# Kernel tuning notes

Measured on AMD Instinct MI355X. Metric: run time of the kernel, lower is better.

The kernel has to match this reference:

```python
import jax, jax.numpy as jnp
import numpy as np
from jax import lax

N_SEEDS = 16
N_SAMPS = 32
IN_C = 3
HID = [32, 64, 64]
K = 3
H = W = 64
EPS = 1e-5


def _uniform(key, shape, bound):
    return jax.random.uniform(key, shape, jnp.float32, -bound, bound)


def setup_inputs() -> dict:
    key = jax.random.key(0)
    keys = jax.random.split(key, 32)
    inp = {"x": jax.random.normal(keys[0], (N_SEEDS, N_SAMPS, IN_C, H, W), jnp.float32)}
    c_in = IN_C
    ki = 1
    for li, c_out in enumerate(HID, start=1):
        fan_in = c_in * K * K
        # kaiming_uniform with a=sqrt(5): gain=sqrt(2/(1+5))=sqrt(1/3); bound=sqrt(3)*gain/sqrt(fan)=1/sqrt(fan)
        wb = 1.0 / np.sqrt(fan_in)
        inp[f"w{li}"] = _uniform(keys[ki], (N_SEEDS * c_out, c_in, K, K), wb); ki += 1
        inp[f"b{li}"] = _uniform(keys[ki], (N_SEEDS * c_out,), wb); ki += 1
        inp[f"g{li}"] = jnp.ones((N_SEEDS * c_out,), jnp.float32)
        inp[f"be{li}"] = jnp.zeros((N_SEEDS * c_out,), jnp.float32)
        c_in = c_out
    return inp


def _layer(h, w, b, g, be):
    # grouped conv: groups = N_SEEDS, OIHW weights, NCHW data, stride 1, pad 1
    h = lax.conv_general_dilated(
        h, w, window_strides=(1, 1), padding=((1, 1), (1, 1)),
        feature_group_count=N_SEEDS,
        dimension_numbers=("NCHW", "OIHW", "NCHW"))
    h = h + b[None, :, None, None]
    # BatchNorm2d, training mode: batch statistics over (N, H, W), biased variance
    mean = jnp.mean(h, axis=(0, 2, 3))
    var = jnp.var(h, axis=(0, 2, 3))
    h = (h - mean[None, :, None, None]) * (g / jnp.sqrt(var + EPS))[None, :, None, None] + be[None, :, None, None]
    return jax.nn.relu(h)


def reference(x, w1, b1, g1, be1, w2, b2, g2, be2, w3, b3, g3, be3):
    S, N, C, Hh, Ww = x.shape  # (n_seeds, n_samps, C, H, W)
    h = jnp.swapaxes(x, 0, 1).reshape(N, S * C, Hh, Ww)
    h = _layer(h, w1, b1, g1, be1)
    h = _layer(h, w2, b2, g2, be2)
    h = _layer(h, w3, b3, g3, be3)
    c_out = HID[-1]
    h = h.reshape(N, S, c_out, Hh, Ww)
    return jnp.swapaxes(h, 0, 1)  # (n_seeds, n_samps, C_out, H, W)
```

## Files before the change

kernel.cpp:

```cpp
#include <hip/hip_runtime.h>
#include <cstddef>
#include <cstdint>

typedef __attribute__((ext_vector_type(8))) _Float16 half8;
typedef __attribute__((ext_vector_type(4))) float f32x4;
typedef _Float16 half_t;

#define NS 16
#define NN 32

static const size_t OFF_H1P = 0;
static const size_t OFF_H2P = 138412032ull;
static const size_t OFF_ZR1 = OFF_H2P + 276824064ull;
static const size_t OFF_ZR2 = OFF_ZR1 + 67584ull;
static const size_t OFF_WT1 = OFF_ZR2 + 135168ull;
static const size_t OFF_WT2 = OFF_WT1 + 55296ull;
static const size_t OFF_WT3 = OFF_WT2 + 589824ull;
static const size_t OFF_SUMS = OFF_WT3 + 1179648ull;
static const size_t OFF_PRM = OFF_SUMS + 20480ull;
static const size_t OFF_TH  = OFF_PRM + 30720ull;

static __device__ __forceinline__ half8 sr8(half8 v, half8 t) {
    half8 r = v + t;
    half8 z = {};
#if defined(__has_builtin) && __has_builtin(__builtin_elementwise_max)
    return __builtin_elementwise_max(r, z);
#else
#pragma unroll
    for (int j = 0; j < 8; ++j) r[j] = r[j] > (_Float16)0 ? r[j] : (_Float16)0;
    return r;
#endif
}

__global__ __launch_bounds__(256) void transform1_k(
    const float* __restrict__ w1, float* __restrict__ wt1)
{
    int idx = blockIdx.x * 256 + threadIdx.x;
    if (idx >= 13824) return;
    int o = idx & 31, tap = (idx >> 5) % 9, ic = (idx / 288) % 3, s = idx / 864;
    wt1[idx] = w1[((s * 32 + o) * 3 + ic) * 9 + tap];
}

__global__ __launch_bounds__(256) void wtrans2_k(
    const float* __restrict__ w2, const float* __restrict__ a1, half_t* __restrict__ wt2)
{
    int idx = blockIdx.x * 256 + threadIdx.x;
    if (idx >= 294912) return;
    int ic = idx & 31, oc = (idx >> 5) & 63, tap = (idx >> 11) % 9, s = idx / 18432;
    wt2[idx] = (half_t)(w2[((s * 64 + oc) * 32 + ic) * 9 + tap] * a1[s * 32 + ic]);
}

__global__ __launch_bounds__(256) void wtrans3_k(
    const float* __restrict__ w3, const float* __restrict__ a2, half_t* __restrict__ wt3)
{
    int idx = blockIdx.x * 256 + threadIdx.x;
    if (idx >= 589824) return;
    int ic = idx & 63, oc = (idx >> 6) & 63, tap = (idx >> 12) % 9, s = idx / 36864;
    wt3[idx] = (half_t)(w3[((s * 64 + oc) * 64 + ic) * 9 + tap] * a2[s * 64 + ic]);
}

__global__ __launch_bounds__(256) void conv1_k(
    const float* __restrict__ x, const float* __restrict__ wt1,
    const float* __restrict__ b1, half_t* __restrict__ h1p,
    float* __restrict__ sums1)
{
    __shared__ float smem[8512];
    float* xt = smem;
    float* bounce = smem;
    float* statsl = smem + 8448;
    const int tile = blockIdx.x, s = blockIdx.y, n = blockIdx.z;
    const int tx = tile & 3, ty = tile >> 2, tid = threadIdx.x;

    for (int i = tid; i < 972; i += 256) {
        int ic = i / 324, rem = i - ic * 324;
        int py = rem / 18, px = rem - py * 18;
        int gy = ty * 16 + py - 1, gx = tx * 16 + px - 1;
        float v = 0.f;
        if ((unsigned)gy < 64u && (unsigned)gx < 64u)
            v = x[(size_t)(((s * NN + n) * 3 + ic) * 64 + gy) * 64 + gx];
        xt[i] = v;
    }
    if (tid < 64) statsl[tid] = 0.f;
    __syncthreads();

    const int px = tid & 15, py = tid >> 4;
    float acc[32];
#pragma unroll
    for (int o = 0; o < 32; ++o) acc[o] = 0.f;
#pragma unroll
    for (int ic = 0; ic < 3; ++ic)
#pragma unroll
        for (int ky = 0; ky < 3; ++ky)
#pragma unroll
            for (int kx = 0; kx < 3; ++kx) {
                float v = xt[ic * 324 + (py + ky) * 18 + px + kx];
                const float* wp = wt1 + ((s * 3 + ic) * 9 + ky * 3 + kx) * 32;
#pragma unroll
                for (int o = 0; o < 32; ++o) acc[o] = fmaf(wp[o], v, acc[o]);
            }
    const float* bp = b1 + s * 32;
#pragma unroll
    for (int o = 0; o < 32; ++o) acc[o] += bp[o];

    const int gy1 = ty * 16 + py, gxp = tx * 16 + px + 1;
    half8* dst = (half8*)(h1p + (size_t)(n * NS + s) * 135168 + (size_t)(gy1 * 66 + gxp) * 32);
#pragma unroll
    for (int k = 0; k < 4; ++k) {
        half8 v8;
#pragma unroll
        for (int j = 0; j < 8; ++j) v8[j] = (half_t)acc[k * 8 + j];
        dst[k] = v8;
    }
    __syncthreads();
#pragma unroll
    for (int o = 0; o < 32; ++o) bounce[tid * 33 + o] = acc[o];
    __syncthreads();
    {
        const int oc = tid & 31, grp = tid >> 5;
        float s1 = 0.f, s2 = 0.f;
#pragma unroll 4
        for (int j = 0; j < 32; ++j) {
            float v = bounce[(grp * 32 + j) * 33 + oc];
            s1 += v; s2 += v * v;
        }
        atomicAdd(&statsl[oc * 2], s1);
        atomicAdd(&statsl[oc * 2 + 1], s2);
    }
    __syncthreads();
    if (tid < 64)
        atomicAdd(&sums1[(s * 32 + (tid >> 1)) * 2 + (tid & 1)], statsl[tid]);
}

__global__ void bnparam_k(const float* __restrict__ sums, const float* __restrict__ g,
                          const float* __restrict__ be, float* __restrict__ a,
                          float* __restrict__ b, float* __restrict__ t,
                          half_t* __restrict__ th, int C)
{
    int ch = blockIdx.x * 256 + threadIdx.x;
    if (ch >= C) return;
    const float inv = 1.f / 131072.f;
    float mean = sums[ch * 2] * inv;
    float var = sums[ch * 2 + 1] * inv - mean * mean;
    float sc = g[ch] * rsqrtf(var + 1e-5f);
    a[ch] = sc;
    float bb = be[ch] - mean * sc;
    b[ch] = bb;
    float tt = bb / sc;
    t[ch] = tt;
    th[ch] = (half_t)tt;
}

__global__ __launch_bounds__(256) void padfill_k(
    half_t* __restrict__ img, half_t* __restrict__ zrow, const float* __restrict__ t,
    int C, int c8shift, long imgstride, int rowstride, long tot_cols, long tot)
{
    long idx = (long)blockIdx.x * 256 + threadIdx.x;
    if (idx >= tot) return;
    const int nc8m = (1 << c8shift) - 1;
    if (idx < tot_cols) {
        int c8 = (int)idx & nc8m; long r = idx >> c8shift;
        int side = (int)r & 1; r >>= 1;
        int y = (int)r & 63; r >>= 6;
        int si = (int)(r & 15); int ni = (int)(r >> 4);
        half8 q;
#pragma unroll
        for (int j = 0; j < 8; ++j) q[j] = (half_t)(-(t[si * C + c8 * 8 + j] + 1.0f));
        *(half8*)(img + (long)(ni * NS + si) * imgstride + (long)y * rowstride +
                  (side ? 65 : 0) * C + c8 * 8) = q;
    } else {
        long r2 = idx - tot_cols;
        int c8 = (int)r2 & nc8m; r2 >>= c8shift;
        int xx = (int)(r2 % 66); int si = (int)(r2 / 66);
        half8 q;
#pragma unroll
        for (int j = 0; j < 8; ++j) q[j] = (half_t)(-(t[si * C + c8 * 8 + j] + 1.0f));
        *(half8*)(zrow + ((long)(si * 66 + xx)) * C + c8 * 8) = q;
    }
}

__device__ __forceinline__ void loadB2(half8 bf[4], const half_t* wb, int tap, int l15, int g) {
#pragma unroll
    for (int nt = 0; nt < 4; ++nt)
        bf[nt] = *(const half8*)(wb + (tap * 64 + nt * 16 + l15) * 32 + g * 8);
}

__device__ __forceinline__ void comp2(f32x4 acc[4][4], const half8 bf[4], const char* smem,
                                      int tap, int wv, int l15, int g) {
    const int ky = tap / 3, kx = tap - ky * 3;
#pragma unroll
    for (int mt = 0; mt < 4; ++mt) {
        int p = (wv * 4 + mt + ky) * 18 + l15 + kx;
        half8 av = *(const half8*)(smem + p * 80 + g * 16);
#pragma unroll
        for (int nt = 0; nt < 4; ++nt)
            acc[mt][nt] = __builtin_amdgcn_mfma_f32_16x16x32_f16(av, bf[nt], acc[mt][nt], 0, 0, 0);
    }
}

__global__ __launch_bounds__(256, 3) void conv2_k(
    const half_t* __restrict__ h1p, const half_t* __restrict__ zr1,
    const half_t* __restrict__ wt2, const float* __restrict__ b2,
    const half_t* __restrict__ th1, half_t* __restrict__ h2p,
    float* __restrict__ sums2)
{
    __shared__ __align__(16) char smem[37376];
    float* statsl = (float*)(smem + 36864);
    const int tile = blockIdx.x, s = blockIdx.y, n = blockIdx.z;
    const int tx = tile & 3, ty = tile >> 2, tid = threadIdx.x;
    const int l = tid & 63, wv = tid >> 6, l15 = l & 15, g = l >> 4;
    if (tid < 128) statsl[tid] = 0.f;

    const half_t* wb = wt2 + (size_t)s * 18432;
    half8 bfa[4], bfb[4];
    loadB2(bfa, wb, 0, l15, g);

    const half_t* img = h1p + (size_t)(n * NS + s) * 135168;
    const half_t* zrow = zr1 + s * 2112;
    const int j = tid & 3;
    const half8 tshj = *(const half8*)(th1 + s * 32 + j * 8);
    for (int i = tid; i < 1296; i += 256) {
        int p = i >> 2;
        int py = p / 18, pxx = p - py * 18;
        int gy = ty * 16 + py - 1;
        const half_t* rp = ((unsigned)gy < 64u) ? (img + (size_t)gy * 2112) : zrow;
        half8 v = sr8(*(const half8*)(rp + (tx * 16 + pxx) * 32 + j * 8), tshj);
        *(half8*)(smem + p * 80 + j * 16) = v;
    }
    __syncthreads();

    f32x4 acc[4][4];
#pragma unroll
    for (int mt = 0; mt < 4; ++mt)
#pragma unroll
        for (int nt = 0; nt < 4; ++nt) acc[mt][nt] = (f32x4){0.f, 0.f, 0.f, 0.f};

#pragma unroll
    for (int tap = 0; tap < 9; ++tap) {
        if (tap & 1) {
            if (tap < 8) loadB2(bfa, wb, tap + 1, l15, g);
            comp2(acc, bfb, smem, tap, wv, l15, g);
        } else {
            if (tap < 8) loadB2(bfb, wb, tap + 1, l15, g);
            comp2(acc, bfa, smem, tap, wv, l15, g);
        }
    }

    float s1a[4], s2a[4];
#pragma unroll
    for (int nt = 0; nt < 4; ++nt) {
        float bias = b2[s * 64 + nt * 16 + l15];
        float s1 = 0.f, s2 = 0.f;
#pragma unroll
        for (int mt = 0; mt < 4; ++mt)
#pragma unroll
            for (int r = 0; r < 4; ++r) {
                float v = acc[mt][nt][r] + bias;
                acc[mt][nt][r] = v;
                s1 += v; s2 += v * v;
            }
        s1 += __shfl_xor(s1, 16); s1 += __shfl_xor(s1, 32);
        s2 += __shfl_xor(s2, 16); s2 += __shfl_xor(s2, 32);
        s1a[nt] = s1; s2a[nt] = s2;
    }
    if (l < 16) {
#pragma unroll
        for (int nt = 0; nt < 4; ++nt) {
            atomicAdd(&statsl[(nt * 16 + l15) * 2], s1a[nt]);
            atomicAdd(&statsl[(nt * 16 + l15) * 2 + 1], s2a[nt]);
        }
    }
    __syncthreads();

    half_t* obuf = (half_t*)smem;
#pragma unroll
    for (int mt = 0; mt < 4; ++mt)
#pragma unroll
        for (int nt = 0; nt < 4; ++nt)
#pragma unroll
            for (int r = 0; r < 4; ++r)
                obuf[((wv * 4 + mt) * 16 + g * 4 + r) * 72 + nt * 16 + l15] = (half_t)acc[mt][nt][r];
    __syncthreads();

    half_t* img2 = h2p + (size_t)(n * NS + s) * 270336;
    for (int i = tid; i < 2048; i += 256) {
        int p = i >> 3, cc = i & 7;
        int y = ty * 16 + (p >> 4), xp = tx * 16 + (p & 15) + 1;
        *(half8*)(img2 + (size_t)y * 4224 + xp * 64 + cc * 8) = *(const half8*)(obuf + p * 72 + cc * 8);
    }
    if (tid < 128)
        atomicAdd(&sums2[(s * 64 + (tid >> 1)) * 2 + (tid & 1)], statsl[tid]);
}

__device__ __forceinline__ void loadB3(half8 bf[2][2], const half_t* wb, int tap,
                                       int och, int l15, int g) {
#pragma unroll
    for (int nt = 0; nt < 2; ++nt) {
        const half_t* r = wb + (tap * 64 + och * 32 + nt * 16 + l15) * 64 + g * 8;
        bf[nt][0] = *(const half8*)(r);
        bf[nt][1] = *(const half8*)(r + 32);
    }
}

__device__ __forceinline__ void comp3(f32x4 acc[4][2], const half8 bf[2][2], const char* smem,
                                      int tap, int wy, int l15, int g) {
    const int ky = tap / 3, kx = tap - ky * 3;
#pragma unroll
    for (int mt = 0; mt < 4; ++mt) {
        int p = (wy + ky) * 66 + mt * 16 + l15 + kx;
        int base = p * 128, sw = (p & 7) << 4;
        half8 a0 = *(const half8*)(smem + base + ((g * 16) ^ sw));
        half8 a1 = *(const half8*)(smem + base + ((64 + g * 16) ^ sw));
#pragma unroll
        for (int nt = 0; nt < 2; ++nt) {
            acc[mt][nt] = __builtin_amdgcn_mfma_f32_16x16x32_f16(a0, bf[nt][0], acc[mt][nt], 0, 0, 0);
            acc[mt][nt] = __builtin_amdgcn_mfma_f32_16x16x32_f16(a1, bf[nt][1], acc[mt][nt], 0, 0, 0);
        }
    }
}

__global__ __launch_bounds__(512, 4) void conv3_k(
    const half_t* __restrict__ h2p, const half_t* __restrict__ zr2,
    const half_t* __restrict__ wt3, const float* __restrict__ b3,
    const half_t* __restrict__ th2, float* __restrict__ out,
    float* __restrict__ sums3)
{
    __shared__ __align__(16) char smem[51200];
    float* statsl = (float*)(smem + 50688);
    const int ty = blockIdx.x, s = blockIdx.y, n = blockIdx.z;
    const int tid = threadIdx.x;
    const int l = tid & 63, w = tid >> 6, l15 = l & 15, g = l >> 4;
    const int wy = w & 3, och = w >> 2;
    if (tid < 128) statsl[tid] = 0.f;

    const half_t* wb = wt3 + (size_t)s * 36864;
    half8 bfa[2][2], bfb[2][2];
    loadB3(bfa, wb, 0, och, l15, g);

    const half_t* img = h2p + (size_t)(n * NS + s) * 270336;
    const half_t* zrow = zr2 + s * 4224;
    const int j = tid & 7;
    const half8 tshj = *(const half8*)(th2 + s * 64 + j * 8);
    for (int i = tid; i < 3168; i += 512) {
        int p = i >> 3;
        int row = p / 66, col = p - row * 66;
        int gy = ty * 4 + row - 1;
        const half_t* rp = ((unsigned)gy < 64u) ? (img + (size_t)gy * 4224) : zrow;
        half8 v = sr8(*(const half8*)(rp + col * 64 + j * 8), tshj);
        *(half8*)(smem + p * 128 + ((j * 16) ^ ((p & 7) << 4))) = v;
    }
    __syncthreads();

    f32x4 acc[4][2];
#pragma unroll
    for (int mt = 0; mt < 4; ++mt)
#pragma unroll
        for (int nt = 0; nt < 2; ++nt) acc[mt][nt] = (f32x4){0.f, 0.f, 0.f, 0.f};

#pragma unroll
    for (int tap = 0; tap < 9; ++tap) {
        if (tap & 1) {
            if (tap < 8) loadB3(bfa, wb, tap + 1, och, l15, g);
            comp3(acc, bfb, smem, tap, wy, l15, g);
        } else {
            if (tap < 8) loadB3(bfb, wb, tap + 1, och, l15, g);
            comp3(acc, bfa, smem, tap, wy, l15, g);
        }
    }

    float s1a[2], s2a[2];
#pragma unroll
    for (int nt = 0; nt < 2; ++nt) {
        float bias = b3[s * 64 + och * 32 + nt * 16 + l15];
        float s1 = 0.f, s2 = 0.f;
#pragma unroll
        for (int mt = 0; mt < 4; ++mt)
#pragma unroll
            for (int r = 0; r < 4; ++r) {
                float v = acc[mt][nt][r] + bias;
                acc[mt][nt][r] = v;
                s1 += v; s2 += v * v;
            }
        s1 += __shfl_xor(s1, 16); s1 += __shfl_xor(s1, 32);
        s2 += __shfl_xor(s2, 16); s2 += __shfl_xor(s2, 32);
        s1a[nt] = s1; s2a[nt] = s2;
    }
    if (l < 16) {
#pragma unroll
        for (int nt = 0; nt < 2; ++nt) {
            atomicAdd(&statsl[(och * 32 + nt * 16 + l15) * 2], s1a[nt]);
            atomicAdd(&statsl[(och * 32 + nt * 16 + l15) * 2 + 1], s2a[nt]);
        }
    }

    const int gy = ty * 4 + wy;
#pragma unroll
    for (int mt = 0; mt < 4; ++mt)
#pragma unroll
        for (int nt = 0; nt < 2; ++nt) {
            int c = och * 32 + nt * 16 + l15;
            *(f32x4*)(out + ((size_t)((s * NN + n) * 64 + c) * 64 + gy) * 64 + mt * 16 + g * 4) = acc[mt][nt];
        }
    __syncthreads();
    if (tid < 128)
        atomicAdd(&sums3[(s * 64 + (tid >> 1)) * 2 + (tid & 1)], statsl[tid]);
}

__global__ __launch_bounds__(256) void final_k(float* __restrict__ out,
                                               const float* __restrict__ a3,
                                               const float* __restrict__ b3p)
{
    size_t i = ((size_t)blockIdx.x * 256 + threadIdx.x) * 4;
    int ch = (int)((i >> 12) & 63) + (int)(i >> 23) * 64;
    float sc = a3[ch], sh = b3p[ch];
    f32x4 v = *(f32x4*)(out + i);
#pragma unroll
    for (int r = 0; r < 4; ++r) v[r] = fmaxf(fmaf(sc, v[r], sh), 0.f);
    *(f32x4*)(out + i) = v;
}

extern "C" void kernel_launch(void* const* d_in, const int* in_sizes, int n_in,
                              void* d_out, int out_size, void* d_ws, size_t ws_size,
                              hipStream_t stream)
{
    const float* x   = (const float*)d_in[0];
    const float* w1  = (const float*)d_in[1];
    const float* b1  = (const float*)d_in[2];
    const float* g1  = (const float*)d_in[3];
    const float* be1 = (const float*)d_in[4];
    const float* w2  = (const float*)d_in[5];
    const float* b2  = (const float*)d_in[6];
    const float* g2  = (const float*)d_in[7];
    const float* be2 = (const float*)d_in[8];
    const float* w3  = (const float*)d_in[9];
    const float* b3  = (const float*)d_in[10];
    const float* g3  = (const float*)d_in[11];
    const float* be3 = (const float*)d_in[12];

    char* ws = (char*)d_ws;
    half_t* h1p = (half_t*)(ws + OFF_H1P);
    half_t* h2p = (half_t*)(ws + OFF_H2P);
    half_t* zr1 = (half_t*)(ws + OFF_ZR1);
    half_t* zr2 = (half_t*)(ws + OFF_ZR2);
    float*  wt1 = (float*)(ws + OFF_WT1);
    half_t* wt2 = (half_t*)(ws + OFF_WT2);
    half_t* wt3 = (half_t*)(ws + OFF_WT3);
    float*  sums = (float*)(ws + OFF_SUMS);
    float *s1v = sums, *s2v = sums + 1024, *s3v = sums + 3072;
    float*  prm = (float*)(ws + OFF_PRM);
    float *a1 = prm,        *b1p = prm + 512,  *t1 = prm + 1024;
    float *a2 = prm + 1536, *b2p = prm + 2560, *t2 = prm + 3584;
    float *a3 = prm + 4608, *b3p = prm + 5632, *t3 = prm + 6656;
    half_t* th = (half_t*)(ws + OFF_TH);
    half_t *th1 = th, *th2 = th + 512, *th3 = th + 1536;
    float* out = (float*)d_out;

    hipMemsetAsync(ws + OFF_SUMS, 0, 20480, stream);
    transform1_k<<<54, 256, 0, stream>>>(w1, wt1);
    dim3 grid(16, 16, 32);
    conv1_k<<<grid, 256, 0, stream>>>(x, wt1, b1, h1p, s1v);
    bnparam_k<<<2, 256, 0, stream>>>(s1v, g1, be1, a1, b1p, t1, th1, 512);
    padfill_k<<<1041, 256, 0, stream>>>(h1p, zr1, t1, 32, 2, 135168L, 2112, 262144L, 266368L);
    wtrans2_k<<<1152, 256, 0, stream>>>(w2, a1, wt2);
    conv2_k<<<grid, 256, 0, stream>>>(h1p, zr1, wt2, b2, th1, h2p, s2v);
    bnparam_k<<<4, 256, 0, stream>>>(s2v, g2, be2, a2, b2p, t2, th2, 1024);
    padfill_k<<<2081, 256, 0, stream>>>(h2p, zr2, t2, 64, 3, 270336L, 4224, 524288L, 532736L);
    wtrans3_k<<<2304, 256, 0, stream>>>(w3, a2, wt3);
    dim3 grid3(16, 16, 32);
    conv3_k<<<grid3, 512, 0, stream>>>(h2p, zr2, wt3, b3, th2, out, s3v);
    bnparam_k<<<4, 256, 0, stream>>>(s3v, g3, be3, a3, b3p, t3, th3, 1024);
    final_k<<<131072, 256, 0, stream>>>(out, a3, b3p);
}
```

Measured before the change: 877.0 us.

## Make conv2/conv3 blocks stream whole images through a rolling row buffer

conv2 and conv3 now launch one block per (sample, seed) image instead of many small tiles. Each block walks all 64 rows in groups of four, keeping an 8-row circular LDS buffer and prefetching the next rows into registers while the current rows compute. This removes the halo rows that were reloaded for every tile and the per-tile setup, at the cost of only 512 blocks (fewer than before) and extra barriers per row group. final_k also becomes a grid-stride loop over a smaller grid.

```diff
diff --git a/kernel.cpp b/kernel.cpp
--- a/kernel.cpp
+++ b/kernel.cpp
@@ -178,115 +178,136 @@
     }
 }
 
-__device__ __forceinline__ void loadB2(half8 bf[4], const half_t* wb, int tap, int l15, int g) {
-#pragma unroll
-    for (int nt = 0; nt < 4; ++nt)
-        bf[nt] = *(const half8*)(wb + (tap * 64 + nt * 16 + l15) * 32 + g * 8);
-}
-
-__device__ __forceinline__ void comp2(f32x4 acc[4][4], const half8 bf[4], const char* smem,
-                                      int tap, int wv, int l15, int g) {
-    const int ky = tap / 3, kx = tap - ky * 3;
+__device__ __forceinline__ void loadB2(half8 bf[2], const half_t* wb, int tap,
+                                       int och, int l15, int g) {
+#pragma unroll
+    for (int nt = 0; nt < 2; ++nt)
+        bf[nt] = *(const half8*)(wb + (tap * 64 + och * 32 + nt * 16 + l15) * 32 + g * 8);
+}
+
+__device__ __forceinline__ void comp2r(f32x4 acc[4][2], const half8 bf[2], const char* smem,
+                                       int row, int kx, int l15, int g) {
+    const char* rowp = smem + (row & 7) * 5280;
 #pragma unroll
     for (int mt = 0; mt < 4; ++mt) {
-        int p = (wv * 4 + mt + ky) * 18 + l15 + kx;
-        half8 av = *(const half8*)(smem + p * 80 + g * 16);
-#pragma unroll
-        for (int nt = 0; nt < 4; ++nt)
+        int p = mt * 16 + l15 + kx;
+        half8 av = *(const half8*)(rowp + p * 80 + g * 16);
+#pragma unroll
+        for (int nt = 0; nt < 2; ++nt)
             acc[mt][nt] = __builtin_amdgcn_mfma_f32_16x16x32_f16(av, bf[nt], acc[mt][nt], 0, 0, 0);
     }
 }
 
-__global__ __launch_bounds__(256, 3) void conv2_k(
+__global__ __launch_bounds__(512, 4) void conv2_k(
     const half_t* __restrict__ h1p, const half_t* __restrict__ zr1,
     const half_t* __restrict__ wt2, const float* __restrict__ b2,
     const half_t* __restrict__ th1, half_t* __restrict__ h2p,
     float* __restrict__ sums2)
 {
-    __shared__ __align__(16) char smem[37376];
-    float* statsl = (float*)(smem + 36864);
-    const int tile = blockIdx.x, s = blockIdx.y, n = blockIdx.z;
-    const int tx = tile & 3, ty = tile >> 2, tid = threadIdx.x;
-    const int l = tid & 63, wv = tid >> 6, l15 = l & 15, g = l >> 4;
+    __shared__ __align__(16) char smem[79616];
+    half_t* obuf = (half_t*)(smem + 42240);
+    float* statsl = (float*)(smem + 79104);
+    const int n = blockIdx.x, s = blockIdx.y;
+    const int tid = threadIdx.x;
+    const int l = tid & 63, w = tid >> 6, l15 = l & 15, g = l >> 4;
+    const int wy = w & 3, och = w >> 2;
     if (tid < 128) statsl[tid] = 0.f;
-
-    const half_t* wb = wt2 + (size_t)s * 18432;
-    half8 bfa[4], bfb[4];
-    loadB2(bfa, wb, 0, l15, g);
 
     const half_t* img = h1p + (size_t)(n * NS + s) * 135168;
     const half_t* zrow = zr1 + s * 2112;
+    const half_t* wb = wt2 + (size_t)s * 18432;
     const int j = tid & 3;
     const half8 tshj = *(const half8*)(th1 + s * 32 + j * 8);
-    for (int i = tid; i < 1296; i += 256) {
+
+    for (int i = tid; i < 1584; i += 512) {
         int p = i >> 2;
-        int py = p / 18, pxx = p - py * 18;
-        int gy = ty * 16 + py - 1;
-        const half_t* rp = ((unsigned)gy < 64u) ? (img + (size_t)gy * 2112) : zrow;
-        half8 v = sr8(*(const half8*)(rp + (tx * 16 + pxx) * 32 + j * 8), tshj);
-        *(half8*)(smem + p * 80 + j * 16) = v;
-    }
-    __syncthreads();
-
-    f32x4 acc[4][4];
-#pragma unroll
-    for (int mt = 0; mt < 4; ++mt)
-#pragma unroll
-        for (int nt = 0; nt < 4; ++nt) acc[mt][nt] = (f32x4){0.f, 0.f, 0.f, 0.f};
-
-#pragma unroll
-    for (int tap = 0; tap < 9; ++tap) {
-        if (tap & 1) {
-            if (tap < 8) loadB2(bfa, wb, tap + 1, l15, g);
-            comp2(acc, bfb, smem, tap, wv, l15, g);
-        } else {
-            if (tap < 8) loadB2(bfb, wb, tap + 1, l15, g);
-            comp2(acc, bfa, smem, tap, wv, l15, g);
+        int rr = p / 66, col = p - rr * 66;
+        int row = rr - 1;
+        const half_t* rp = (row < 0) ? zrow : (img + (size_t)row * 2112);
+        half8 v = sr8(*(const half8*)(rp + col * 32 + j * 8), tshj);
+        *(half8*)(smem + (row & 7) * 5280 + col * 80 + j * 16) = v;
+    }
+    __syncthreads();
+
+    float bias0 = b2[s * 64 + och * 32 + l15];
+    float bias1 = b2[s * 64 + och * 32 + 16 + l15];
+    float s1a0 = 0.f, s1a1 = 0.f, s2a0 = 0.f, s2a1 = 0.f;
+    half_t* img2 = h2p + (size_t)(n * NS + s) * 270336;
+
+    half8 bfa[2], bfb[2];
+#pragma unroll 1
+    for (int t = 0; t < 16; ++t) {
+        const int rowbase = 4 * t + 5;
+        half8 st0, st1, st2;
+        int sl0, sl1, sl2;
+#define PREP2(K, ST, SL) { int idx = tid + K * 512; int p = idx >> 2; int rr = p / 66; \
+        int col = p - rr * 66; int row = rowbase + rr; bool ok = (idx < 1056) && (row <= 64); \
+        const half_t* rp = (row >= 64) ? zrow : (img + (size_t)row * 2112); \
+        ST = *(const half8*)(rp + col * 32 + j * 8); \
+        SL = ok ? ((row & 7) * 5280 + col * 80 + j * 16) : -1; }
+        PREP2(0, st0, sl0)
+        PREP2(1, st1, sl1)
+        PREP2(2, st2, sl2)
+#undef PREP2
+
+        f32x4 acc[4][2];
+#pragma unroll
+        for (int mt = 0; mt < 4; ++mt)
+#pragma unroll
+            for (int nt = 0; nt < 2; ++nt) acc[mt][nt] = (f32x4){0.f, 0.f, 0.f, 0.f};
+
+        const int gy = 4 * t + wy;
+        loadB2(bfa, wb, 0, och, l15, g);
+#pragma unroll
+        for (int tap = 0; tap < 9; ++tap) {
+            int ky = tap / 3, kx = tap - ky * 3;
+            if (tap & 1) {
+                if (tap < 8) loadB2(bfa, wb, tap + 1, och, l15, g);
+                comp2r(acc, bfb, smem, gy - 1 + ky, kx, l15, g);
+            } else {
+                if (tap < 8) loadB2(bfb, wb, tap + 1, och, l15, g);
+                comp2r(acc, bfa, smem, gy - 1 + ky, kx, l15, g);
+            }
         }
-    }
-
-    float s1a[4], s2a[4];
-#pragma unroll
-    for (int nt = 0; nt < 4; ++nt) {
-        float bias = b2[s * 64 + nt * 16 + l15];
-        float s1 = 0.f, s2 = 0.f;
+
+        __syncthreads();
+        if (sl0 >= 0) *(half8*)(smem + sl0) = sr8(st0, tshj);
+        if (sl1 >= 0) *(half8*)(smem + sl1) = sr8(st1, tshj);
+        if (sl2 >= 0) *(half8*)(smem + sl2) = sr8(st2, tshj);
 #pragma unroll
         for (int mt = 0; mt < 4; ++mt)
 #pragma unroll
-            for (int r = 0; r < 4; ++r) {
-                float v = acc[mt][nt][r] + bias;
-                acc[mt][nt][r] = v;
-                s1 += v; s2 += v * v;
+            for (int nt = 0; nt < 2; ++nt) {
+                f32x4 v = acc[mt][nt];
+                float bias = nt ? bias1 : bias0;
+#pragma unroll
+                for (int r = 0; r < 4; ++r) {
+                    float vv = v[r] + bias;
+                    if (nt) { s1a1 += vv; s2a1 += vv * vv; } else { s1a0 += vv; s2a0 += vv * vv; }
+                    obuf[(wy * 64 + mt * 16 + g * 4 + r) * 72 + och * 32 + nt * 16 + l15] = (half_t)vv;
+                }
             }
-        s1 += __shfl_xor(s1, 16); s1 += __shfl_xor(s1, 32);
-        s2 += __shfl_xor(s2, 16); s2 += __shfl_xor(s2, 32);
-        s1a[nt] = s1; s2a[nt] = s2;
-    }
+        __syncthreads();
+
+        for (int i = tid; i < 2048; i += 512) {
+            int c8 = i & 7, p = i >> 3;
+            int lr = p >> 6, xx = p & 63;
+            *(half8*)(img2 + (size_t)(4 * t + lr) * 4224 + (xx + 1) * 64 + c8 * 8) =
+                *(const half8*)(obuf + p * 72 + c8 * 8);
+        }
+    }
+
+    s1a0 += __shfl_xor(s1a0, 16); s1a0 += __shfl_xor(s1a0, 32);
+    s2a0 += __shfl_xor(s2a0, 16); s2a0 += __shfl_xor(s2a0, 32);
+    s1a1 += __shfl_xor(s1a1, 16); s1a1 += __shfl_xor(s1a1, 32);
+    s2a1 += __shfl_xor(s2a1, 16); s2a1 += __shfl_xor(s2a1, 32);
     if (l < 16) {
-#pragma unroll
-        for (int nt = 0; nt < 4; ++nt) {
-            atomicAdd(&statsl[(nt * 16 + l15) * 2], s1a[nt]);
-            atomicAdd(&statsl[(nt * 16 + l15) * 2 + 1], s2a[nt]);
-        }
-    }
-    __syncthreads();
-
-    half_t* obuf = (half_t*)smem;
-#pragma unroll
-    for (int mt = 0; mt < 4; ++mt)
-#pragma unroll
-        for (int nt = 0; nt < 4; ++nt)
-#pragma unroll
-            for (int r = 0; r < 4; ++r)
-                obuf[((wv * 4 + mt) * 16 + g * 4 + r) * 72 + nt * 16 + l15] = (half_t)acc[mt][nt][r];
-    __syncthreads();
-
-    half_t* img2 = h2p + (size_t)(n * NS + s) * 270336;
-    for (int i = tid; i < 2048; i += 256) {
-        int p = i >> 3, cc = i & 7;
-        int y = ty * 16 + (p >> 4), xp = tx * 16 + (p & 15) + 1;
-        *(half8*)(img2 + (size_t)y * 4224 + xp * 64 + cc * 8) = *(const half8*)(obuf + p * 72 + cc * 8);
-    }
+        atomicAdd(&statsl[(och * 32 + l15) * 2], s1a0);
+        atomicAdd(&statsl[(och * 32 + l15) * 2 + 1], s2a0);
+        atomicAdd(&statsl[(och * 32 + 16 + l15) * 2], s1a1);
+        atomicAdd(&statsl[(och * 32 + 16 + l15) * 2 + 1], s2a1);
+    }
+    __syncthreads();
     if (tid < 128)
         atomicAdd(&sums2[(s * 64 + (tid >> 1)) * 2 + (tid & 1)], statsl[tid]);
 }
@@ -301,15 +322,15 @@
     }
 }
 
-__device__ __forceinline__ void comp3(f32x4 acc[4][2], const half8 bf[2][2], const char* smem,
-                                      int tap, int wy, int l15, int g) {
-    const int ky = tap / 3, kx = tap - ky * 3;
+__device__ __forceinline__ void comp3r(f32x4 acc[4][2], const half8 bf[2][2], const char* smem,
+                                       int row, int kx, int l15, int g) {
+    const char* rowp = smem + (row & 7) * 8448;
 #pragma unroll
     for (int mt = 0; mt < 4; ++mt) {
-        int p = (wy + ky) * 66 + mt * 16 + l15 + kx;
+        int p = mt * 16 + l15 + kx;
         int base = p * 128, sw = (p & 7) << 4;
-        half8 a0 = *(const half8*)(smem + base + ((g * 16) ^ sw));
-        half8 a1 = *(const half8*)(smem + base + ((64 + g * 16) ^ sw));
+        half8 a0 = *(const half8*)(rowp + base + ((g * 16) ^ sw));
+        half8 a1 = *(const half8*)(rowp + base + ((64 + g * 16) ^ sw));
 #pragma unroll
         for (int nt = 0; nt < 2; ++nt) {
             acc[mt][nt] = __builtin_amdgcn_mfma_f32_16x16x32_f16(a0, bf[nt][0], acc[mt][nt], 0, 0, 0);
@@ -324,82 +345,109 @@
     const half_t* __restrict__ th2, float* __restrict__ out,
     float* __restrict__ sums3)
 {
-    __shared__ __align__(16) char smem[51200];
-    float* statsl = (float*)(smem + 50688);
-    const int ty = blockIdx.x, s = blockIdx.y, n = blockIdx.z;
+    __shared__ __align__(16) char smem[68096];
+    float* statsl = (float*)(smem + 67584);
+    const int n = blockIdx.x, s = blockIdx.y;
     const int tid = threadIdx.x;
     const int l = tid & 63, w = tid >> 6, l15 = l & 15, g = l >> 4;
     const int wy = w & 3, och = w >> 2;
     if (tid < 128) statsl[tid] = 0.f;
 
-    const half_t* wb = wt3 + (size_t)s * 36864;
-    half8 bfa[2][2], bfb[2][2];
-    loadB3(bfa, wb, 0, och, l15, g);
-
     const half_t* img = h2p + (size_t)(n * NS + s) * 270336;
     const half_t* zrow = zr2 + s * 4224;
+    const half_t* wb = wt3 + (size_t)s * 36864;
     const int j = tid & 7;
     const half8 tshj = *(const half8*)(th2 + s * 64 + j * 8);
+
     for (int i = tid; i < 3168; i += 512) {
         int p = i >> 3;
-        int row = p / 66, col = p - row * 66;
-        int gy = ty * 4 + row - 1;
-        const half_t* rp = ((unsigned)gy < 64u) ? (img + (size_t)gy * 4224) : zrow;
+        int rr = p / 66, col = p - rr * 66;
+        int row = rr - 1;
+        const half_t* rp = (row < 0) ? zrow : (img + (size_t)row * 4224);
         half8 v = sr8(*(const half8*)(rp + col * 64 + j * 8), tshj);
-        *(half8*)(smem + p * 128 + ((j * 16) ^ ((p & 7) << 4))) = v;
-    }
-    __syncthreads();
-
-    f32x4 acc[4][2];
-#pragma unroll
-    for (int mt = 0; mt < 4; ++mt)
-#pragma unroll
-        for (int nt = 0; nt < 2; ++nt) acc[mt][nt] = (f32x4){0.f, 0.f, 0.f, 0.f};
-
-#pragma unroll
-    for (int tap = 0; tap < 9; ++tap) {
-        if (tap & 1) {
-            if (tap < 8) loadB3(bfa, wb, tap + 1, och, l15, g);
-            comp3(acc, bfb, smem, tap, wy, l15, g);
-        } else {
-            if (tap < 8) loadB3(bfb, wb, tap + 1, och, l15, g);
-            comp3(acc, bfa, smem, tap, wy, l15, g);
+        *(half8*)(smem + (row & 7) * 8448 + col * 128 + ((j * 16) ^ ((col & 7) << 4))) = v;
+    }
+    __syncthreads();
+
+    float bias0 = b3[s * 64 + och * 32 + l15];
+    float bias1 = b3[s * 64 + och * 32 + 16 + l15];
+    float s1a0 = 0.f, s1a1 = 0.f, s2a0 = 0.f, s2a1 = 0.f;
+    const size_t obase = (size_t)((s * NN + n) * 64) * 4096;
+
+    half8 bfa[2][2], bfb[2][2];
+#pragma unroll 1
+    for (int t = 0; t < 16; ++t) {
+        const int rowbase = 4 * t + 5;
+        half8 st0, st1, st2, st3, st4;
+        int sl0, sl1, sl2, sl3, sl4;
+#define PREP3(K, ST, SL) { int idx = tid + K * 512; int p = idx >> 3; int rr = p / 66; \
+        int col = p - rr * 66; int row = rowbase + rr; bool ok = (idx < 2112) && (row <= 64); \
+        const half_t* rp = (row >= 64) ? zrow : (img + (size_t)row * 4224); \
+        ST = *(const half8*)(rp + col * 64 + j * 8); \
+        SL = ok ? ((row & 7) * 8448 + col * 128 + ((j * 16) ^ ((col & 7) << 4))) : -1; }
+        PREP3(0, st0, sl0)
+        PREP3(1, st1, sl1)
+        PREP3(2, st2, sl2)
+        PREP3(3, st3, sl3)
+        PREP3(4, st4, sl4)
+#undef PREP3
+
+        f32x4 acc[4][2];
+#pragma unroll
+        for (int mt = 0; mt < 4; ++mt)
+#pragma unroll
+            for (int nt = 0; nt < 2; ++nt) acc[mt][nt] = (f32x4){0.f, 0.f, 0.f, 0.f};
+
+        const int gy = 4 * t + wy;
+        loadB3(bfa, wb, 0, och, l15, g);
+#pragma unroll
+        for (int tap = 0; tap < 9; ++tap) {
+            int ky = tap / 3, kx = tap - ky * 3;
+            if (tap & 1) {
+                if (tap < 8) loadB3(bfa, wb, tap + 1, och, l15, g);
+                comp3r(acc, bfb, smem, gy - 1 + ky, kx, l15, g);
+            } else {
+                if (tap < 8) loadB3(bfb, wb, tap + 1, och, l15, g);
+                comp3r(acc, bfa, smem, gy - 1 + ky, kx, l15, g);
+            }
         }
-    }
-
-    float s1a[2], s2a[2];
-#pragma unroll
-    for (int nt = 0; nt < 2; ++nt) {
-        float bias = b3[s * 64 + och * 32 + nt * 16 + l15];
-        float s1 = 0.f, s2 = 0.f;
-#pragma unroll
-        for (int mt = 0; mt < 4; ++mt)
-#pragma unroll
-            for (int r = 0; r < 4; ++r) {
-                float v = acc[mt][nt][r] + bias;
-                acc[mt][nt][r] = v;
-                s1 += v; s2 += v * v;
-            }
-        s1 += __shfl_xor(s1, 16); s1 += __shfl_xor(s1, 32);
-        s2 += __shfl_xor(s2, 16); s2 += __shfl_xor(s2, 32);
-        s1a[nt] = s1; s2a[nt] = s2;
-    }
-    if (l < 16) {
-#pragma unroll
-        for (int nt = 0; nt < 2; ++nt) {
-            atomicAdd(&statsl[(och * 32 + nt * 16 + l15) * 2], s1a[nt]);
-            atomicAdd(&statsl[(och * 32 + nt * 16 + l15) * 2 + 1], s2a[nt]);
-        }
-    }
-
-    const int gy = ty * 4 + wy;
-#pragma unroll
-    for (int mt = 0; mt < 4; ++mt)
+
 #pragma unroll
         for (int nt = 0; nt < 2; ++nt) {
             int c = och * 32 + nt * 16 + l15;
-            *(f32x4*)(out + ((size_t)((s * NN + n) * 64 + c) * 64 + gy) * 64 + mt * 16 + g * 4) = acc[mt][nt];
+            float bias = nt ? bias1 : bias0;
+#pragma unroll
+            for (int mt = 0; mt < 4; ++mt) {
+                f32x4 v = acc[mt][nt];
+#pragma unroll
+                for (int r = 0; r < 4; ++r) {
+                    float vv = v[r] + bias;
+                    v[r] = vv;
+                    if (nt) { s1a1 += vv; s2a1 += vv * vv; } else { s1a0 += vv; s2a0 += vv * vv; }
+                }
+                *(f32x4*)(out + obase + (size_t)c * 4096 + gy * 64 + mt * 16 + g * 4) = v;
+            }
         }
+
+        __syncthreads();
+        if (sl0 >= 0) *(half8*)(smem + sl0) = sr8(st0, tshj);
+        if (sl1 >= 0) *(half8*)(smem + sl1) = sr8(st1, tshj);
+        if (sl2 >= 0) *(half8*)(smem + sl2) = sr8(st2, tshj);
+        if (sl3 >= 0) *(half8*)(smem + sl3) = sr8(st3, tshj);
+        if (sl4 >= 0) *(half8*)(smem + sl4) = sr8(st4, tshj);
+        __syncthreads();
+    }
+
+    s1a0 += __shfl_xor(s1a0, 16); s1a0 += __shfl_xor(s1a0, 32);
+    s2a0 += __shfl_xor(s2a0, 16); s2a0 += __shfl_xor(s2a0, 32);
+    s1a1 += __shfl_xor(s1a1, 16); s1a1 += __shfl_xor(s1a1, 32);
+    s2a1 += __shfl_xor(s2a1, 16); s2a1 += __shfl_xor(s2a1, 32);
+    if (l < 16) {
+        atomicAdd(&statsl[(och * 32 + l15) * 2], s1a0);
+        atomicAdd(&statsl[(och * 32 + l15) * 2 + 1], s2a0);
+        atomicAdd(&statsl[(och * 32 + 16 + l15) * 2], s1a1);
+        atomicAdd(&statsl[(och * 32 + 16 + l15) * 2 + 1], s2a1);
+    }
     __syncthreads();
     if (tid < 128)
         atomicAdd(&sums3[(s * 64 + (tid >> 1)) * 2 + (tid & 1)], statsl[tid]);
@@ -409,13 +457,16 @@
                                                const float* __restrict__ a3,
                                                const float* __restrict__ b3p)
 {
-    size_t i = ((size_t)blockIdx.x * 256 + threadIdx.x) * 4;
-    int ch = (int)((i >> 12) & 63) + (int)(i >> 23) * 64;
-    float sc = a3[ch], sh = b3p[ch];
-    f32x4 v = *(f32x4*)(out + i);
-#pragma unroll
-    for (int r = 0; r < 4; ++r) v[r] = fmaxf(fmaf(sc, v[r], sh), 0.f);
-    *(f32x4*)(out + i) = v;
+    const size_t stride = (size_t)gridDim.x * 256;
+    for (size_t i = (size_t)blockIdx.x * 256 + threadIdx.x; i < 33554432ull; i += stride) {
+        size_t e = i * 4;
+        int ch = (int)((e >> 12) & 63) + (int)(e >> 23) * 64;
+        float sc = a3[ch], sh = b3p[ch];
+        f32x4 v = *(f32x4*)(out + e);
+#pragma unroll
+        for (int r = 0; r < 4; ++r) v[r] = fmaxf(fmaf(sc, v[r], sh), 0.f);
+        *(f32x4*)(out + e) = v;
+    }
 }
 
 extern "C" void kernel_launch(void* const* d_in, const int* in_sizes, int n_in,
@@ -456,17 +507,17 @@
 
     hipMemsetAsync(ws + OFF_SUMS, 0, 20480, stream);
     transform1_k<<<54, 256, 0, stream>>>(w1, wt1);
-    dim3 grid(16, 16, 32);
-    conv1_k<<<grid, 256, 0, stream>>>(x, wt1, b1, h1p, s1v);
+    dim3 grid1(16, 16, 32);
+    conv1_k<<<grid1, 256, 0, stream>>>(x, wt1, b1, h1p, s1v);
     bnparam_k<<<2, 256, 0, stream>>>(s1v, g1, be1, a1, b1p, t1, th1, 512);
     padfill_k<<<1041, 256, 0, stream>>>(h1p, zr1, t1, 32, 2, 135168L, 2112, 262144L, 266368L);
     wtrans2_k<<<1152, 256, 0, stream>>>(w2, a1, wt2);
-    conv2_k<<<grid, 256, 0, stream>>>(h1p, zr1, wt2, b2, th1, h2p, s2v);
+    dim3 gridr(32, 16);
+    conv2_k<<<gridr, 512, 0, stream>>>(h1p, zr1, wt2, b2, th1, h2p, s2v);
     bnparam_k<<<4, 256, 0, stream>>>(s2v, g2, be2, a2, b2p, t2, th2, 1024);
     padfill_k<<<2081, 256, 0, stream>>>(h2p, zr2, t2, 64, 3, 270336L, 4224, 524288L, 532736L);
     wtrans3_k<<<2304, 256, 0, stream>>>(w3, a2, wt3);
-    dim3 grid3(16, 16, 32);
-    conv3_k<<<grid3, 512, 0, stream>>>(h2p, zr2, wt3, b3, th2, out, s3v);
+    conv3_k<<<gridr, 512, 0, stream>>>(h2p, zr2, wt3, b3, th2, out, s3v);
     bnparam_k<<<4, 256, 0, stream>>>(s3v, g3, be3, a3, b3p, t3, th3, 1024);
-    final_k<<<131072, 256, 0, stream>>>(out, a3, b3p);
-}
+    final_k<<<4096, 256, 0, stream>>>(out, a3, b3p);
+}
```

Measured after the change: 1.298 ms. 48.0% more time.

## Split layer-3 input channels into two halves to shrink LDS and overlap staging

Applied to the files above, without the earlier changes.

Intermediate h2 is stored as two 32-channel planes instead of one interleaved 64-channel image, with matching changes to the conv2 store and a new padfill3 kernel. conv3 now stages one 32-channel half in LDS at a time, loading the second half into registers while the first half's MFMAs run. This cuts LDS from about 51 KB to 32 KB and raises the launch-bounds occupancy hint from 4 to 6. Bias and statistics are now fused into the output store, and final_k becomes a grid-stride loop with fewer blocks. The costs are extra barriers, more register pressure from the prefetched halves, and dropping the XOR swizzle in favour of an 80-byte padded stride.

```diff
diff --git a/kernel.cpp b/kernel.cpp
--- a/kernel.cpp
+++ b/kernel.cpp
@@ -119,8 +119,8 @@
         const int oc = tid & 31, grp = tid >> 5;
         float s1 = 0.f, s2 = 0.f;
 #pragma unroll 4
-        for (int j = 0; j < 32; ++j) {
-            float v = bounce[(grp * 32 + j) * 33 + oc];
+        for (int jj = 0; jj < 32; ++jj) {
+            float v = bounce[(grp * 32 + jj) * 33 + oc];
             s1 += v; s2 += v * v;
         }
         atomicAdd(&statsl[oc * 2], s1);
@@ -178,6 +178,34 @@
     }
 }
 
+__global__ __launch_bounds__(256) void padfill3_k(
+    half_t* __restrict__ h2p, half_t* __restrict__ zr2, const float* __restrict__ t)
+{
+    int idx = blockIdx.x * 256 + threadIdx.x;
+    if (idx >= 532736) return;
+    if (idx < 524288) {
+        int c8 = idx & 3; int r = idx >> 2;
+        int side = r & 1; r >>= 1;
+        int y = r & 63; r >>= 6;
+        int kc = r & 1; r >>= 1;
+        int si = r & 15; int ni = r >> 4;
+        half8 q;
+#pragma unroll
+        for (int j = 0; j < 8; ++j) q[j] = (half_t)(-(t[si * 64 + kc * 32 + c8 * 8 + j] + 1.0f));
+        *(half8*)(h2p + (size_t)(ni * NS + si) * 270336 + kc * 135168 +
+                  (size_t)y * 2112 + (side ? 65 : 0) * 32 + c8 * 8) = q;
+    } else {
+        int r2 = idx - 524288;
+        int c8 = r2 & 3; r2 >>= 2;
+        int xx = r2 % 66; r2 /= 66;
+        int kc = r2 & 1; int si = r2 >> 1;
+        half8 q;
+#pragma unroll
+        for (int j = 0; j < 8; ++j) q[j] = (half_t)(-(t[si * 64 + kc * 32 + c8 * 8 + j] + 1.0f));
+        *(half8*)(zr2 + si * 4224 + kc * 2112 + xx * 32 + c8 * 8) = q;
+    }
+}
+
 __device__ __forceinline__ void loadB2(half8 bf[4], const half_t* wb, int tap, int l15, int g) {
 #pragma unroll
     for (int nt = 0; nt < 4; ++nt)
@@ -283,72 +311,61 @@
 
     half_t* img2 = h2p + (size_t)(n * NS + s) * 270336;
     for (int i = tid; i < 2048; i += 256) {
-        int p = i >> 3, cc = i & 7;
+        int c8 = i & 3, p = (i >> 2) & 255, kc = i >> 10;
         int y = ty * 16 + (p >> 4), xp = tx * 16 + (p & 15) + 1;
-        *(half8*)(img2 + (size_t)y * 4224 + xp * 64 + cc * 8) = *(const half8*)(obuf + p * 72 + cc * 8);
+        *(half8*)(img2 + kc * 135168 + (size_t)y * 2112 + xp * 32 + c8 * 8) =
+            *(const half8*)(obuf + p * 72 + kc * 32 + c8 * 8);
     }
     if (tid < 128)
         atomicAdd(&sums2[(s * 64 + (tid >> 1)) * 2 + (tid & 1)], statsl[tid]);
 }
 
-__device__ __forceinline__ void loadB3(half8 bf[2][2], const half_t* wb, int tap,
-                                       int och, int l15, int g) {
-#pragma unroll
-    for (int nt = 0; nt < 2; ++nt) {
-        const half_t* r = wb + (tap * 64 + och * 32 + nt * 16 + l15) * 64 + g * 8;
-        bf[nt][0] = *(const half8*)(r);
-        bf[nt][1] = *(const half8*)(r + 32);
-    }
-}
-
-__device__ __forceinline__ void comp3(f32x4 acc[4][2], const half8 bf[2][2], const char* smem,
-                                      int tap, int wy, int l15, int g) {
-    const int ky = tap / 3, kx = tap - ky * 3;
-#pragma unroll
-    for (int mt = 0; mt < 4; ++mt) {
-        int p = (wy + ky) * 66 + mt * 16 + l15 + kx;
-        int base = p * 128, sw = (p & 7) << 4;
-        half8 a0 = *(const half8*)(smem + base + ((g * 16) ^ sw));
-        half8 a1 = *(const half8*)(smem + base + ((64 + g * 16) ^ sw));
-#pragma unroll
-        for (int nt = 0; nt < 2; ++nt) {
-            acc[mt][nt] = __builtin_amdgcn_mfma_f32_16x16x32_f16(a0, bf[nt][0], acc[mt][nt], 0, 0, 0);
-            acc[mt][nt] = __builtin_amdgcn_mfma_f32_16x16x32_f16(a1, bf[nt][1], acc[mt][nt], 0, 0, 0);
-        }
-    }
-}
-
-__global__ __launch_bounds__(512, 4) void conv3_k(
+__global__ __launch_bounds__(512, 6) void conv3_k(
     const half_t* __restrict__ h2p, const half_t* __restrict__ zr2,
     const half_t* __restrict__ wt3, const float* __restrict__ b3,
     const half_t* __restrict__ th2, float* __restrict__ out,
     float* __restrict__ sums3)
 {
-    __shared__ __align__(16) char smem[51200];
-    float* statsl = (float*)(smem + 50688);
+    __shared__ __align__(16) char smem[32192];
+    float* statsl = (float*)(smem + 31680);
     const int ty = blockIdx.x, s = blockIdx.y, n = blockIdx.z;
     const int tid = threadIdx.x;
     const int l = tid & 63, w = tid >> 6, l15 = l & 15, g = l >> 4;
     const int wy = w & 3, och = w >> 2;
+    const int ty4 = ty * 4;
     if (tid < 128) statsl[tid] = 0.f;
 
+    const half_t* img0 = h2p + (size_t)(n * NS + s) * 270336;
+    const half_t* img1 = img0 + 135168;
+    const half_t* zr0 = zr2 + s * 4224;
+    const half_t* zr1p = zr0 + 2112;
     const half_t* wb = wt3 + (size_t)s * 36864;
-    half8 bfa[2][2], bfb[2][2];
-    loadB3(bfa, wb, 0, och, l15, g);
-
-    const half_t* img = h2p + (size_t)(n * NS + s) * 270336;
-    const half_t* zrow = zr2 + s * 4224;
-    const int j = tid & 7;
-    const half8 tshj = *(const half8*)(th2 + s * 64 + j * 8);
-    for (int i = tid; i < 3168; i += 512) {
-        int p = i >> 3;
-        int row = p / 66, col = p - row * 66;
-        int gy = ty * 4 + row - 1;
-        const half_t* rp = ((unsigned)gy < 64u) ? (img + (size_t)gy * 4224) : zrow;
-        half8 v = sr8(*(const half8*)(rp + col * 64 + j * 8), tshj);
-        *(half8*)(smem + p * 128 + ((j * 16) ^ ((p & 7) << 4))) = v;
-    }
-    __syncthreads();
+    const int j = tid & 3;
+    const half8 tsh0 = *(const half8*)(th2 + s * 64 + j * 8);
+    const half8 tsh1 = *(const half8*)(th2 + s * 64 + 32 + j * 8);
+
+    half8 sa0, sa1, sa2, sa3; int aa0, aa1, aa2, aa3;
+#define PREP(K, ST, SL, IMG, ZR) { int idx = tid + K * 512; int p = idx >> 2; int rr = p / 66; \
+    int col = p - rr * 66; int row = ty4 - 1 + rr; bool okk = idx < 1584; \
+    const half_t* rp = ((unsigned)row < 64u) ? ((IMG) + (size_t)row * 2112) : (ZR); \
+    ST = *(const half8*)(rp + col * 32 + j * 8); \
+    SL = okk ? (rr * 5280 + col * 80 + j * 16) : -1; }
+    PREP(0, sa0, aa0, img0, zr0)
+    PREP(1, sa1, aa1, img0, zr0)
+    PREP(2, sa2, aa2, img0, zr0)
+    PREP(3, sa3, aa3, img0, zr0)
+    if (aa0 >= 0) *(half8*)(smem + aa0) = sr8(sa0, tsh0);
+    if (aa1 >= 0) *(half8*)(smem + aa1) = sr8(sa1, tsh0);
+    if (aa2 >= 0) *(half8*)(smem + aa2) = sr8(sa2, tsh0);
+    if (aa3 >= 0) *(half8*)(smem + aa3) = sr8(sa3, tsh0);
+    __syncthreads();
+
+    half8 sb0, sb1, sb2, sb3; int ab0, ab1, ab2, ab3;
+    PREP(0, sb0, ab0, img1, zr1p)
+    PREP(1, sb1, ab1, img1, zr1p)
+    PREP(2, sb2, ab2, img1, zr1p)
+    PREP(3, sb3, ab3, img1, zr1p)
+#undef PREP
 
     f32x4 acc[4][2];
 #pragma unroll
@@ -356,50 +373,93 @@
 #pragma unroll
         for (int nt = 0; nt < 2; ++nt) acc[mt][nt] = (f32x4){0.f, 0.f, 0.f, 0.f};
 
-#pragma unroll
-    for (int tap = 0; tap < 9; ++tap) {
-        if (tap & 1) {
-            if (tap < 8) loadB3(bfa, wb, tap + 1, och, l15, g);
-            comp3(acc, bfb, smem, tap, wy, l15, g);
-        } else {
-            if (tap < 8) loadB3(bfb, wb, tap + 1, och, l15, g);
-            comp3(acc, bfa, smem, tap, wy, l15, g);
-        }
-    }
-
-    float s1a[2], s2a[2];
-#pragma unroll
-    for (int nt = 0; nt < 2; ++nt) {
-        float bias = b3[s * 64 + och * 32 + nt * 16 + l15];
-        float s1 = 0.f, s2 = 0.f;
-#pragma unroll
-        for (int mt = 0; mt < 4; ++mt)
-#pragma unroll
-            for (int r = 0; r < 4; ++r) {
-                float v = acc[mt][nt][r] + bias;
-                acc[mt][nt][r] = v;
-                s1 += v; s2 += v * v;
-            }
-        s1 += __shfl_xor(s1, 16); s1 += __shfl_xor(s1, 32);
-        s2 += __shfl_xor(s2, 16); s2 += __shfl_xor(s2, 32);
-        s1a[nt] = s1; s2a[nt] = s2;
-    }
-    if (l < 16) {
-#pragma unroll
-        for (int nt = 0; nt < 2; ++nt) {
-            atomicAdd(&statsl[(och * 32 + nt * 16 + l15) * 2], s1a[nt]);
-            atomicAdd(&statsl[(och * 32 + nt * 16 + l15) * 2 + 1], s2a[nt]);
-        }
-    }
-
-    const int gy = ty * 4 + wy;
+    half8 bqa[2], bqb[2];
+#define LWA(TAP, KC) { \
+    bqa[0] = *(const half8*)(wb + ((TAP) * 64 + och * 32 + l15) * 64 + (KC) * 32 + g * 8); \
+    bqa[1] = *(const half8*)(wb + ((TAP) * 64 + och * 32 + 16 + l15) * 64 + (KC) * 32 + g * 8); }
+#define LWB(TAP, KC) { \
+    bqb[0] = *(const half8*)(wb + ((TAP) * 64 + och * 32 + l15) * 64 + (KC) * 32 + g * 8); \
+    bqb[1] = *(const half8*)(wb + ((TAP) * 64 + och * 32 + 16 + l15) * 64 + (KC) * 32 + g * 8); }
+#define CSA(KY, KX) { const char* rp_ = smem + (wy + (KY)) * 5280; \
+    _Pragma("unroll") \
+    for (int mt = 0; mt < 4; ++mt) { \
+        int px = mt * 16 + l15 + (KX); \
+        half8 a_ = *(const half8*)(rp_ + px * 80 + g * 16); \
+        acc[mt][0] = __builtin_amdgcn_mfma_f32_16x16x32_f16(a_, bqa[0], acc[mt][0], 0, 0, 0); \
+        acc[mt][1] = __builtin_amdgcn_mfma_f32_16x16x32_f16(a_, bqa[1], acc[mt][1], 0, 0, 0); \
+    } }
+#define CSB(KY, KX) { const char* rp_ = smem + (wy + (KY)) * 5280; \
+    _Pragma("unroll") \
+    for (int mt = 0; mt < 4; ++mt) { \
+        int px = mt * 16 + l15 + (KX); \
+        half8 a_ = *(const half8*)(rp_ + px * 80 + g * 16); \
+        acc[mt][0] = __builtin_amdgcn_mfma_f32_16x16x32_f16(a_, bqb[0], acc[mt][0], 0, 0, 0); \
+        acc[mt][1] = __builtin_amdgcn_mfma_f32_16x16x32_f16(a_, bqb[1], acc[mt][1], 0, 0, 0); \
+    } }
+
+    LWA(0, 0)
+    LWB(1, 0)  CSA(0, 0)
+    LWA(2, 0)  CSB(0, 1)
+    LWB(3, 0)  CSA(0, 2)
+    LWA(4, 0)  CSB(1, 0)
+    LWB(5, 0)  CSA(1, 1)
+    LWA(6, 0)  CSB(1, 2)
+    LWB(7, 0)  CSA(2, 0)
+    LWA(8, 0)  CSB(2, 1)
+    LWB(0, 1)  CSA(2, 2)
+    __syncthreads();
+
+    if (ab0 >= 0) *(half8*)(smem + ab0) = sr8(sb0, tsh1);
+    if (ab1 >= 0) *(half8*)(smem + ab1) = sr8(sb1, tsh1);
+    if (ab2 >= 0) *(half8*)(smem + ab2) = sr8(sb2, tsh1);
+    if (ab3 >= 0) *(half8*)(smem + ab3) = sr8(sb3, tsh1);
+    __syncthreads();
+
+    LWA(1, 1)  CSB(0, 0)
+    LWB(2, 1)  CSA(0, 1)
+    LWA(3, 1)  CSB(0, 2)
+    LWB(4, 1)  CSA(1, 0)
+    LWA(5, 1)  CSB(1, 1)
+    LWB(6, 1)  CSA(1, 2)
+    LWA(7, 1)  CSB(2, 0)
+    LWB(8, 1)  CSA(2, 1)
+               CSB(2, 2)
+#undef CSA
+#undef CSB
+#undef LWA
+#undef LWB
+
+    float bias0 = b3[s * 64 + och * 32 + l15];
+    float bias1 = b3[s * 64 + och * 32 + 16 + l15];
+    float s10 = 0.f, s20 = 0.f, s11 = 0.f, s21 = 0.f;
+    const int gy = ty4 + wy;
+    float* obase = out + (size_t)((s * NN + n) * 64) * 4096;
 #pragma unroll
     for (int mt = 0; mt < 4; ++mt)
 #pragma unroll
         for (int nt = 0; nt < 2; ++nt) {
             int c = och * 32 + nt * 16 + l15;
-            *(f32x4*)(out + ((size_t)((s * NN + n) * 64 + c) * 64 + gy) * 64 + mt * 16 + g * 4) = acc[mt][nt];
+            f32x4 v = acc[mt][nt];
+            float bias = nt ? bias1 : bias0;
+#pragma unroll
+            for (int r = 0; r < 4; ++r) {
+                float vv = v[r] + bias;
+                v[r] = vv;
+                if (nt) { s11 += vv; s21 += vv * vv; } else { s10 += vv; s20 += vv * vv; }
+            }
+            *(f32x4*)(obase + (size_t)c * 4096 + gy * 64 + mt * 16 + g * 4) = v;
         }
+
+    s10 += __shfl_xor(s10, 16); s10 += __shfl_xor(s10, 32);
+    s20 += __shfl_xor(s20, 16); s20 += __shfl_xor(s20, 32);
+    s11 += __shfl_xor(s11, 16); s11 += __shfl_xor(s11, 32);
+    s21 += __shfl_xor(s21, 16); s21 += __shfl_xor(s21, 32);
+    if (l < 16) {
+        atomicAdd(&statsl[(och * 32 + l15) * 2], s10);
+        atomicAdd(&statsl[(och * 32 + l15) * 2 + 1], s20);
+        atomicAdd(&statsl[(och * 32 + 16 + l15) * 2], s11);
+        atomicAdd(&statsl[(och * 32 + 16 + l15) * 2 + 1], s21);
+    }
     __syncthreads();
     if (tid < 128)
         atomicAdd(&sums3[(s * 64 + (tid >> 1)) * 2 + (tid & 1)], statsl[tid]);
@@ -409,13 +469,16 @@
                                                const float* __restrict__ a3,
                                                const float* __restrict__ b3p)
 {
-    size_t i = ((size_t)blockIdx.x * 256 + threadIdx.x) * 4;
-    int ch = (int)((i >> 12) & 63) + (int)(i >> 23) * 64;
-    float sc = a3[ch], sh = b3p[ch];
-    f32x4 v = *(f32x4*)(out + i);
-#pragma unroll
-    for (int r = 0; r < 4; ++r) v[r] = fmaxf(fmaf(sc, v[r], sh), 0.f);
-    *(f32x4*)(out + i) = v;
+    const size_t stride = (size_t)gridDim.x * 256;
+    for (size_t i = (size_t)blockIdx.x * 256 + threadIdx.x; i < 33554432ull; i += stride) {
+        size_t e = i * 4;
+        int ch = (int)((e >> 12) & 63) + (int)(e >> 23) * 64;
+        float sc = a3[ch], sh = b3p[ch];
+        f32x4 v = *(f32x4*)(out + e);
+#pragma unroll
+        for (int r = 0; r < 4; ++r) v[r] = fmaxf(fmaf(sc, v[r], sh), 0.f);
+        *(f32x4*)(out + e) = v;
+    }
 }
 
 extern "C" void kernel_launch(void* const* d_in, const int* in_sizes, int n_in,
@@ -456,17 +519,17 @@
 
     hipMemsetAsync(ws + OFF_SUMS, 0, 20480, stream);
     transform1_k<<<54, 256, 0, stream>>>(w1, wt1);
-    dim3 grid(16, 16, 32);
-    conv1_k<<<grid, 256, 0, stream>>>(x, wt1, b1, h1p, s1v);
+    dim3 grid1(16, 16, 32);
+    conv1_k<<<grid1, 256, 0, stream>>>(x, wt1, b1, h1p, s1v);
     bnparam_k<<<2, 256, 0, stream>>>(s1v, g1, be1, a1, b1p, t1, th1, 512);
     padfill_k<<<1041, 256, 0, stream>>>(h1p, zr1, t1, 32, 2, 135168L, 2112, 262144L, 266368L);
     wtrans2_k<<<1152, 256, 0, stream>>>(w2, a1, wt2);
-    conv2_k<<<grid, 256, 0, stream>>>(h1p, zr1, wt2, b2, th1, h2p, s2v);
+    conv2_k<<<grid1, 256, 0, stream>>>(h1p, zr1, wt2, b2, th1, h2p, s2v);
     bnparam_k<<<4, 256, 0, stream>>>(s2v, g2, be2, a2, b2p, t2, th2, 1024);
-    padfill_k<<<2081, 256, 0, stream>>>(h2p, zr2, t2, 64, 3, 270336L, 4224, 524288L, 532736L);
+    padfill3_k<<<2081, 256, 0, stream>>>(h2p, zr2, t2);
     wtrans3_k<<<2304, 256, 0, stream>>>(w3, a2, wt3);
     dim3 grid3(16, 16, 32);
     conv3_k<<<grid3, 512, 0, stream>>>(h2p, zr2, wt3, b3, th2, out, s3v);
     bnparam_k<<<4, 256, 0, stream>>>(s3v, g3, be3, a3, b3p, t3, th3, 1024);
-    final_k<<<131072, 256, 0, stream>>>(out, a3, b3p);
-}
+    final_k<<<4096, 256, 0, stream>>>(out, a3, b3p);
+}
```

Result: slower. 1.052 ms (+20.0%).
